# Performance work log

Hardware: AMD Instinct MI355X
Metric: run time of the kernel (lower is better)

## Reference

```python
import jax, jax.numpy as jnp
import numpy as np

HEADS = 4
DIM_HEAD = 32
GROUPS = 32  # min(256//4, 32)
EPS = 1e-5


def setup_inputs() -> dict:
    key = jax.random.key(0)
    ks = jax.random.split(key, 6)
    B, C, H, W = 16, 256, 64, 64
    hidden = HEADS * DIM_HEAD  # 128
    return {
        "x": jax.random.normal(ks[0], (B, C, H, W), dtype=jnp.float32),
        "gn_w": jax.random.uniform(ks[1], (C,), dtype=jnp.float32),
        "gn_b": jax.random.normal(ks[2], (C,), dtype=jnp.float32) * 0.05,
        "qkv_w": jax.random.normal(ks[3], (3 * hidden, C), dtype=jnp.float32) * 0.05,
        "qkv_b": jax.random.normal(ks[4], (3 * hidden,), dtype=jnp.float32) * 0.05,
        "out_w": jax.random.normal(ks[5], (C, hidden), dtype=jnp.float32) * 0.05,
        "out_b": jnp.zeros((C,), dtype=jnp.float32),
    }


def _forward_single(x, gn_w, gn_b, qkv_w, qkv_b, out_w, out_b):
    # x: (c, h, w)
    c, h, w = x.shape
    # GroupNorm over (channels-in-group, h, w)
    xg = x.reshape(GROUPS, c // GROUPS, h, w)
    mean = xg.mean(axis=(1, 2, 3), keepdims=True)
    var = xg.var(axis=(1, 2, 3), keepdims=True)
    xn = ((xg - mean) * jax.lax.rsqrt(var + EPS)).reshape(c, h, w)
    xn = xn * gn_w[:, None, None] + gn_b[:, None, None]
    # 1x1 conv QKV projection
    qkv = jnp.einsum('oc,chw->ohw', qkv_w, xn) + qkv_b[:, None, None]
    qkv = qkv.reshape(3, HEADS, DIM_HEAD, h * w)
    q, k, v = qkv[0], qkv[1], qkv[2]
    k = jax.nn.softmax(k, axis=-1)  # softmax over spatial
    context = jnp.einsum('hdn,hen->hde', k, v)   # (heads, d, d)
    out = jnp.einsum('hde,hdn->hen', context, q)  # (heads, d, n)
    out = out.reshape(HEADS * DIM_HEAD, h, w)
    # 1x1 conv output projection
    return jnp.einsum('oc,chw->ohw', out_w, out) + out_b[:, None, None]


def reference(x, gn_w, gn_b, qkv_w, qkv_b, out_w, out_b):
    f = lambda xi: _forward_single(xi, gn_w, gn_b, qkv_w, qkv_b, out_w, out_b)
    return jax.vmap(f)(x)
```

## Files before the change

kernel.cpp:

```cpp
#include <hip/hip_runtime.h>
#include <stdint.h>

typedef unsigned short u16;
typedef __attribute__((ext_vector_type(8))) short bf16x8;
typedef __attribute__((ext_vector_type(4))) float f32x4;

#define B_   16
#define C_   256
#define HW_  4096
#define QR_  384
#define HID_ 128

__device__ __forceinline__ float b2f(u16 u) {
  union { uint32_t i; float f; } v; v.i = ((uint32_t)u) << 16; return v.f;
}
__device__ __forceinline__ u16 f2b(float f) {
  union { float f; uint32_t i; } v; v.f = f;
  uint32_t r = (v.i + 0x7FFFu + ((v.i >> 16) & 1u)) >> 16;
  return (u16)r;
}

__global__ __launch_bounds__(256) void gn_stats_conv_kernel(
    const float* __restrict__ x, const float* __restrict__ gnw,
    const float* __restrict__ gnb, float* __restrict__ scale,
    float* __restrict__ shiftv,
    const float* __restrict__ qkvw, u16* __restrict__ cqkvw,
    u16* __restrict__ wqT)
{
  if (blockIdx.x >= 512) {
    int bi = blockIdx.x - 512;
    int t = threadIdx.x;
    if (bi < 96) {
      int i = bi * 256 + t;
      float4 f = ((const float4*)qkvw)[i];
      ushort4 o;
      o.x = f2b(f.x); o.y = f2b(f.y); o.z = f2b(f.z); o.w = f2b(f.w);
      ((ushort4*)cqkvw)[i] = o;
      return;
    }
    __shared__ u16 tl[16][272];
    for (int j = 0; j < 8; ++j) {
      int d = j * 16 + (t >> 4);
      int cb = (t & 15) * 16;
#pragma unroll
      for (int ii = 0; ii < 16; ++ii)
        tl[t >> 4][cb + ii] = f2b(qkvw[(size_t)d * 256 + cb + ii]);
      __syncthreads();
      union { u16 v[16]; uint4 q[2]; } pk;
#pragma unroll
      for (int dd = 0; dd < 16; ++dd) pk.v[dd] = tl[dd][t];
      *(uint4*)(wqT + (size_t)t * 128 + j * 16)     = pk.q[0];
      *(uint4*)(wqT + (size_t)t * 128 + j * 16 + 8) = pk.q[1];
      __syncthreads();
    }
    return;
  }
  int b = blockIdx.x >> 5, g = blockIdx.x & 31;
  const float* p = x + ((size_t)b * C_ + g * 8) * HW_;
  int t = threadIdx.x;
  float s = 0.f, sq = 0.f;
#pragma unroll
  for (int i = 0; i < 16; ++i) {
    float4 u0 = *(const float4*)(p + t * 8 + i * 2048);
    float4 u1 = *(const float4*)(p + t * 8 + i * 2048 + 4);
    s  += u0.x + u0.y + u0.z + u0.w + u1.x + u1.y + u1.z + u1.w;
    sq += u0.x*u0.x + u0.y*u0.y + u0.z*u0.z + u0.w*u0.w
        + u1.x*u1.x + u1.y*u1.y + u1.z*u1.z + u1.w*u1.w;
  }
#pragma unroll
  for (int off = 32; off > 0; off >>= 1) {
    s  += __shfl_down(s, off);
    sq += __shfl_down(sq, off);
  }
  __shared__ float ps[4], pq[4], mr[2];
  int lane = t & 63, w = t >> 6;
  if (lane == 0) { ps[w] = s; pq[w] = sq; }
  __syncthreads();
  if (t == 0) {
    float S = ps[0] + ps[1] + ps[2] + ps[3];
    float Q = pq[0] + pq[1] + pq[2] + pq[3];
    float mean = S * (1.f / 32768.f);
    float var  = Q * (1.f / 32768.f) - mean * mean;
    mr[0] = mean; mr[1] = rsqrtf(var + 1e-5f);
  }
  __syncthreads();
  if (t < 8) {
    int c = g * 8 + t;
    float sc = gnw[c] * mr[1];
    scale[b * C_ + c]  = sc;
    shiftv[b * C_ + c] = gnb[c] - mr[0] * sc;
  }
}

__global__ __launch_bounds__(256) void gn_transpose_kernel(
    const float* __restrict__ x, u16* __restrict__ dst,
    const float* __restrict__ scale, const float* __restrict__ shiftv)
{
  int nt = blockIdx.x, ct = blockIdx.y, b = blockIdx.z;
  const float* S = x + (size_t)b * C_ * HW_;
  u16* D = dst + (size_t)b * HW_ * C_;
  __shared__ __align__(16) u16 tile[64][136];
  int t = threadIdx.x;
  int n0 = nt * 128, c0 = ct * 64;
  int r = t >> 2, seg = (t & 3) * 32;
  float sc = scale[(size_t)b * C_ + c0 + r];
  float sh = shiftv[(size_t)b * C_ + c0 + r];
#pragma unroll
  for (int i = 0; i < 4; ++i) {
    const float* rp = S + (size_t)(c0 + r) * HW_ + n0 + seg + i * 8;
    float4 u0 = *(const float4*)(rp);
    float4 u1 = *(const float4*)(rp + 4);
    float f[8] = {u0.x, u0.y, u0.z, u0.w, u1.x, u1.y, u1.z, u1.w};
    uint4 o;
    uint32_t* op = (uint32_t*)&o;
#pragma unroll
    for (int j = 0; j < 4; ++j) {
      op[j] = (uint32_t)f2b(f[2 * j] * sc + sh)
            | ((uint32_t)f2b(f[2 * j + 1] * sc + sh) << 16);
    }
    *(uint4*)&tile[r][seg + i * 8] = o;
  }
  __syncthreads();
#pragma unroll
  for (int i = 0; i < 4; ++i) {
    int m = t * 4 + i;
    int n_l = m >> 3, cg = (m & 7) * 8;
    union { u16 v[8]; uint4 q; } pk;
#pragma unroll
    for (int e = 0; e < 8; ++e) pk.v[e] = tile[cg + e][n_l];
    *(uint4*)(D + (size_t)(n0 + n_l) * C_ + c0 + cg) = pk.q;
  }
}

__global__ __launch_bounds__(512) void kv_ctx_kernel(
    const u16* __restrict__ A,
    const u16* __restrict__ Bt,
    float* __restrict__ ctx_part,
    float* __restrict__ s_part)
{
  const int K = C_;
  int nt = blockIdx.x, b = blockIdx.y;
  const u16* Ab = A;
  const u16* Bb = Bt + (size_t)b * HW_ * C_ + (size_t)nt * 128 * K;
  __shared__ __align__(16) union {
    struct { u16 lA[256 * 64]; u16 lB[128 * 64]; } st;
    struct { u16 ek[128][136]; u16 vv[128][136]; float sred[2][128]; } ep;
    float cred[4096];
  } sm;
  int t = threadIdx.x;
  int lane = t & 63, w = t >> 6;
  int quad = lane >> 4, l16 = lane & 15;
  int wm = (w >> 1) * 64, wn = (w & 1) * 64;
  f32x4 acc[4][4];
#pragma unroll
  for (int i = 0; i < 4; ++i)
#pragma unroll
    for (int j = 0; j < 4; ++j)
#pragma unroll
      for (int r = 0; r < 4; ++r) acc[i][j][r] = 0.f;

  for (int k0 = 0; k0 < K; k0 += 64) {
    __syncthreads();
#pragma unroll
    for (int q = 0; q < 4; ++q) {
      int ch = q * 512 + t;
      int row = ch >> 3, off = (ch & 7) * 8;
      __builtin_amdgcn_global_load_lds(
          (const __attribute__((address_space(1))) void*)(Ab + (size_t)row * K + k0 + off),
          (__attribute__((address_space(3))) void*)(sm.st.lA + ch * 8), 16, 0, 0);
    }
#pragma unroll
    for (int q = 0; q < 2; ++q) {
      int ch = q * 512 + t;
      int row = ch >> 3, off = (ch & 7) * 8;
      __builtin_amdgcn_global_load_lds(
          (const __attribute__((address_space(1))) void*)(Bb + (size_t)row * K + k0 + off),
          (__attribute__((address_space(3))) void*)(sm.st.lB + ch * 8), 16, 0, 0);
    }
    __syncthreads();
    const bf16x8* A8 = (const bf16x8*)sm.st.lA;
    const bf16x8* B8 = (const bf16x8*)sm.st.lB;
#pragma unroll
    for (int kk = 0; kk < 2; ++kk) {
      bf16x8 af[4], bfr[4];
#pragma unroll
      for (int i = 0; i < 4; ++i) af[i]  = A8[(wm + i * 16 + l16) * 8 + kk * 4 + quad];
#pragma unroll
      for (int j = 0; j < 4; ++j) bfr[j] = B8[(wn + j * 16 + l16) * 8 + kk * 4 + quad];
#pragma unroll
      for (int i = 0; i < 4; ++i)
#pragma unroll
        for (int j = 0; j < 4; ++j)
          acc[i][j] = __builtin_amdgcn_mfma_f32_16x16x32_bf16(af[i], bfr[j],
                                                              acc[i][j], 0, 0, 0);
    }
  }

  __syncthreads();
  int h = w >> 1, nh = w & 1;
  if (w < 4) {
    float sl[4][4];
#pragma unroll
    for (int i = 0; i < 4; ++i)
#pragma unroll
      for (int r = 0; r < 4; ++r) sl[i][r] = 0.f;
#pragma unroll
    for (int i = 0; i < 4; ++i)
#pragma unroll
      for (int j = 0; j < 4; ++j)
#pragma unroll
        for (int r = 0; r < 4; ++r) {
          float e = __expf(acc[i][j][r]);
          sl[i][r] += e;
          sm.ep.ek[wm + i * 16 + quad * 4 + r][wn + j * 16 + l16] = f2b(e);
        }
#pragma unroll
    for (int i = 0; i < 4; ++i)
#pragma unroll
      for (int r = 0; r < 4; ++r) {
        float v = sl[i][r];
        v += __shfl_xor(v, 1);
        v += __shfl_xor(v, 2);
        v += __shfl_xor(v, 4);
        v += __shfl_xor(v, 8);
        if (l16 == 0) sm.ep.sred[nh][wm + i * 16 + quad * 4 + r] = v;
      }
  } else {
#pragma unroll
    for (int i = 0; i < 4; ++i)
#pragma unroll
      for (int j = 0; j < 4; ++j)
#pragma unroll
        for (int r = 0; r < 4; ++r)
          sm.ep.vv[wm - 128 + i * 16 + quad * 4 + r][wn + j * 16 + l16] =
              f2b(acc[i][j][r]);
  }
  __syncthreads();
  if (t < 128)
    s_part[((size_t)b * 32 + nt) * 128 + t] = sm.ep.sred[0][t] + sm.ep.sred[1][t];

  f32x4 c2[2][2];
#pragma unroll
  for (int i = 0; i < 2; ++i)
#pragma unroll
    for (int j = 0; j < 2; ++j)
#pragma unroll
      for (int r = 0; r < 4; ++r) c2[i][j][r] = 0.f;
#pragma unroll
  for (int kk = 0; kk < 2; ++kk) {
    bf16x8 ae[2], be[2];
#pragma unroll
    for (int i = 0; i < 2; ++i)
      ae[i] = *(const bf16x8*)&sm.ep.ek[h * 32 + i * 16 + l16][nh * 64 + kk * 32 + quad * 8];
#pragma unroll
    for (int j = 0; j < 2; ++j)
      be[j] = *(const bf16x8*)&sm.ep.vv[h * 32 + j * 16 + l16][nh * 64 + kk * 32 + quad * 8];
#pragma unroll
    for (int i = 0; i < 2; ++i)
#pragma unroll
      for (int j = 0; j < 2; ++j)
        c2[i][j] = __builtin_amdgcn_mfma_f32_16x16x32_bf16(ae[i], be[j], c2[i][j], 0, 0, 0);
  }
  __syncthreads();
  if (nh == 0) {
#pragma unroll
    for (int i = 0; i < 2; ++i)
#pragma unroll
      for (int j = 0; j < 2; ++j)
#pragma unroll
        for (int r = 0; r < 4; ++r)
          sm.cred[h * 1024 + (i * 16 + quad * 4 + r) * 32 + j * 16 + l16] = c2[i][j][r];
  }
  __syncthreads();
  if (nh == 1) {
#pragma unroll
    for (int i = 0; i < 2; ++i)
#pragma unroll
      for (int j = 0; j < 2; ++j)
#pragma unroll
        for (int r = 0; r < 4; ++r)
          sm.cred[h * 1024 + (i * 16 + quad * 4 + r) * 32 + j * 16 + l16] += c2[i][j][r];
  }
  __syncthreads();
  float4* dst = (float4*)(ctx_part + ((size_t)b * 32 + nt) * 4096);
  const float4* src4 = (const float4*)sm.cred;
  dst[t] = src4[t];
  dst[t + 512] = src4[t + 512];
}

__global__ __launch_bounds__(256) void fold_kernel(
    const float* __restrict__ ctx_part, const float* __restrict__ s_part,
    const float* __restrict__ outw, const float* __restrict__ qkvb,
    u16* __restrict__ wf, float* __restrict__ btp)
{
  int b = blockIdx.x >> 2, h = blockIdx.x & 3;
  int t = threadIdx.x;
  __shared__ float cs[1024];
  __shared__ float sinv[32];
  const float* cp = ctx_part + ((size_t)b * 32) * 4096 + h * 1024;
  float4 aa = make_float4(0.f, 0.f, 0.f, 0.f);
  for (int ntb = 0; ntb < 32; ++ntb) {
    float4 v = *(const float4*)(cp + (size_t)ntb * 4096 + t * 4);
    aa.x += v.x; aa.y += v.y; aa.z += v.z; aa.w += v.w;
  }
  *(float4*)&cs[t * 4] = aa;
  if (t < 32) {
    float ssum = 0.f;
    for (int ntb = 0; ntb < 32; ++ntb)
      ssum += s_part[((size_t)b * 32 + ntb) * 128 + h * 32 + t];
    sinv[t] = 1.f / ssum;
  }
  __syncthreads();
  int o = t;
  const float* wr = outw + (size_t)o * HID_ + h * 32;
  float wv[32];
  float cb = 0.f;
#pragma unroll
  for (int e = 0; e < 32; ++e) {
    wv[e] = wr[e];
    cb += wv[e] * qkvb[256 + h * 32 + e];
  }
  union { u16 v[32]; uint4 q[4]; } pk;
  float bacc = 0.f;
#pragma unroll
  for (int d = 0; d < 32; ++d) {
    float a = 0.f;
#pragma unroll
    for (int e = 0; e < 32; ++e) a += wv[e] * cs[d * 32 + e];
    float val = a * sinv[d] + cb;
    pk.v[d] = f2b(val);
    bacc += val * qkvb[h * 32 + d];
  }
  uint4* dp = (uint4*)(wf + ((size_t)b * C_ + o) * HID_ + h * 32);
#pragma unroll
  for (int i = 0; i < 4; ++i) dp[i] = pk.q[i];
  btp[((size_t)b * 4 + h) * 256 + o] = bacc;
}

__global__ __launch_bounds__(256) void out_gemm_kernel(
    const u16* __restrict__ wfp, const u16* __restrict__ wqT,
    const u16* __restrict__ Bt, const float* __restrict__ outb,
    const float* __restrict__ btp, float* __restrict__ Cout)
{
  int nt = blockIdx.x, mt = blockIdx.y, b = blockIdx.z;
  const u16* wfB = wfp + (size_t)b * C_ * HID_ + (size_t)mt * 128 * HID_;
  const u16* Bb  = Bt + (size_t)b * HW_ * C_ + (size_t)nt * 128 * C_;
  __shared__ __align__(16) u16 lWF[128 * 128];
  __shared__ __align__(16) u16 lWQ[64 * 128];
  __shared__ __align__(16) u16 lA[128 * 64];
  __shared__ __align__(16) u16 lB[128 * 64];
  int t = threadIdx.x;
  int lane = t & 63, w = t >> 6;
  int quad = lane >> 4, l16 = lane & 15;
  int wm = (w >> 1) * 64, wn = (w & 1) * 64;

#pragma unroll
  for (int q = 0; q < 8; ++q) {
    int ch = q * 256 + t;
    int row = ch >> 4, off = (ch & 15) * 8;
    __builtin_amdgcn_global_load_lds(
        (const __attribute__((address_space(1))) void*)(wfB + (size_t)row * HID_ + off),
        (__attribute__((address_space(3))) void*)(lWF + ch * 8), 16, 0, 0);
  }
  f32x4 acc[4][4];
#pragma unroll
  for (int i = 0; i < 4; ++i)
#pragma unroll
    for (int j = 0; j < 4; ++j)
#pragma unroll
      for (int r = 0; r < 4; ++r) acc[i][j][r] = 0.f;

  for (int k0 = 0; k0 < C_; k0 += 64) {
    __syncthreads();
#pragma unroll
    for (int q = 0; q < 4; ++q) {
      int ch = q * 256 + t;
      int row = ch >> 4, off = (ch & 15) * 8;
      __builtin_amdgcn_global_load_lds(
          (const __attribute__((address_space(1))) void*)(wqT + (size_t)(k0 + row) * HID_ + off),
          (__attribute__((address_space(3))) void*)(lWQ + ch * 8), 16, 0, 0);
    }
#pragma unroll
    for (int q = 0; q < 4; ++q) {
      int ch = q * 256 + t;
      int row = ch >> 3, off = (ch & 7) * 8;
      __builtin_amdgcn_global_load_lds(
          (const __attribute__((address_space(1))) void*)(Bb + (size_t)row * C_ + k0 + off),
          (__attribute__((address_space(3))) void*)(lB + ch * 8), 16, 0, 0);
    }
    __syncthreads();
    {
      f32x4 facc[2][4];
#pragma unroll
      for (int i2 = 0; i2 < 2; ++i2)
#pragma unroll
        for (int j2 = 0; j2 < 4; ++j2)
#pragma unroll
          for (int r = 0; r < 4; ++r) facc[i2][j2][r] = 0.f;
      const bf16x8* WF8 = (const bf16x8*)lWF;
      const bf16x8* WQ8 = (const bf16x8*)lWQ;
#pragma unroll
      for (int kk = 0; kk < 4; ++kk) {
        bf16x8 afv[2], bfv[4];
#pragma unroll
        for (int i2 = 0; i2 < 2; ++i2)
          afv[i2] = WF8[(w * 32 + i2 * 16 + l16) * 16 + kk * 4 + quad];
#pragma unroll
        for (int j2 = 0; j2 < 4; ++j2)
          bfv[j2] = WQ8[(j2 * 16 + l16) * 16 + kk * 4 + quad];
#pragma unroll
        for (int i2 = 0; i2 < 2; ++i2)
#pragma unroll
          for (int j2 = 0; j2 < 4; ++j2)
            facc[i2][j2] = __builtin_amdgcn_mfma_f32_16x16x32_bf16(
                afv[i2], bfv[j2], facc[i2][j2], 0, 0, 0);
      }
#pragma unroll
      for (int i2 = 0; i2 < 2; ++i2)
#pragma unroll
        for (int j2 = 0; j2 < 4; ++j2)
#pragma unroll
          for (int r = 0; r < 4; ++r)
            lA[(w * 32 + i2 * 16 + quad * 4 + r) * 64 + j2 * 16 + l16] =
                f2b(facc[i2][j2][r]);
    }
    __syncthreads();
    const bf16x8* A8 = (const bf16x8*)lA;
    const bf16x8* B8 = (const bf16x8*)lB;
#pragma unroll
    for (int kk = 0; kk < 2; ++kk) {
      bf16x8 af[4], bfr[4];
#pragma unroll
      for (int i = 0; i < 4; ++i) af[i]  = A8[(wm + i * 16 + l16) * 8 + kk * 4 + quad];
#pragma unroll
      for (int j = 0; j < 4; ++j) bfr[j] = B8[(wn + j * 16 + l16) * 8 + kk * 4 + quad];
#pragma unroll
      for (int i = 0; i < 4; ++i)
#pragma unroll
        for (int j = 0; j < 4; ++j)
          acc[i][j] = __builtin_amdgcn_mfma_f32_16x16x32_bf16(af[i], bfr[j],
                                                              acc[i][j], 0, 0, 0);
    }
  }
#pragma unroll
  for (int i = 0; i < 4; ++i) {
#pragma unroll
    for (int rg = 0; rg < 4; ++rg) {
      int o = mt * 128 + wm + i * 16 + quad * 4 + rg;
      float bsv = outb[o]
                + btp[((size_t)b * 4 + 0) * 256 + o]
                + btp[((size_t)b * 4 + 1) * 256 + o]
                + btp[((size_t)b * 4 + 2) * 256 + o]
                + btp[((size_t)b * 4 + 3) * 256 + o];
      size_t rowbase = (size_t)b * C_ * HW_ + (size_t)o * HW_;
#pragma unroll
      for (int j = 0; j < 4; ++j) {
        int n = nt * 128 + wn + j * 16 + l16;
        Cout[rowbase + n] = acc[i][j][rg] + bsv;
      }
    }
  }
}

extern "C" void kernel_launch(void* const* d_in, const int* in_sizes, int n_in,
                              void* d_out, int out_size, void* d_ws, size_t ws_size,
                              hipStream_t stream)
{
  const float* x    = (const float*)d_in[0];
  const float* gnw  = (const float*)d_in[1];
  const float* gnb  = (const float*)d_in[2];
  const float* qkvw = (const float*)d_in[3];
  const float* qkvb = (const float*)d_in[4];
  const float* outw = (const float*)d_in[5];
  const float* outb = (const float*)d_in[6];

  char* p = (char*)d_ws;
  float* scale  = (float*)p;            p += (size_t)B_ * C_ * 4;
  float* shiftv = (float*)p;            p += (size_t)B_ * C_ * 4;
  u16* cqkvw = (u16*)p;                 p += (size_t)QR_ * C_ * 2;
  u16* wqT   = (u16*)p;                 p += (size_t)C_ * HID_ * 2;
  u16* xn_t  = (u16*)p;                 p += (size_t)B_ * HW_ * C_ * 2;
  u16* wf    = (u16*)p;                 p += (size_t)B_ * C_ * HID_ * 2;
  float* ctxp = (float*)p;              p += (size_t)B_ * 32 * 4 * 1024 * 4;
  float* sp   = (float*)p;              p += (size_t)B_ * 32 * 128 * 4;
  float* btp  = (float*)p;

  gn_stats_conv_kernel<<<609, 256, 0, stream>>>(x, gnw, gnb, scale, shiftv,
                                                qkvw, cqkvw, wqT);
  gn_transpose_kernel<<<dim3(32, 4, 16), 256, 0, stream>>>(x, xn_t, scale, shiftv);
  kv_ctx_kernel<<<dim3(32, 16), 512, 0, stream>>>(cqkvw + 128 * C_, xn_t, ctxp, sp);
  fold_kernel<<<64, 256, 0, stream>>>(ctxp, sp, outw, qkvb, wf, btp);
  out_gemm_kernel<<<dim3(32, 2, 16), 256, 0, stream>>>(wf, wqT, xn_t, outb, btp,
                                                       (float*)d_out);
}
```

Before: 214.9 us.

## Precompute per-batch combined weight in separate GEMM instead of recomputing per tile

After: 195.1 us. -9.2%, faster.

```diff
diff --git a/kernel.cpp b/kernel.cpp
--- a/kernel.cpp
+++ b/kernel.cpp
@@ -337,31 +337,20 @@
   btp[((size_t)b * 4 + h) * 256 + o] = bacc;
 }
 
-__global__ __launch_bounds__(256) void out_gemm_kernel(
+__global__ __launch_bounds__(256) void wtot_gemm_kernel(
     const u16* __restrict__ wfp, const u16* __restrict__ wqT,
-    const u16* __restrict__ Bt, const float* __restrict__ outb,
-    const float* __restrict__ btp, float* __restrict__ Cout)
-{
+    u16* __restrict__ wtot)
+{
+  const int K = HID_;
   int nt = blockIdx.x, mt = blockIdx.y, b = blockIdx.z;
-  const u16* wfB = wfp + (size_t)b * C_ * HID_ + (size_t)mt * 128 * HID_;
-  const u16* Bb  = Bt + (size_t)b * HW_ * C_ + (size_t)nt * 128 * C_;
-  __shared__ __align__(16) u16 lWF[128 * 128];
-  __shared__ __align__(16) u16 lWQ[64 * 128];
+  const u16* Ab = wfp + (size_t)b * C_ * HID_ + (size_t)mt * 128 * K;
+  const u16* Bb = wqT + (size_t)nt * 128 * K;
   __shared__ __align__(16) u16 lA[128 * 64];
   __shared__ __align__(16) u16 lB[128 * 64];
   int t = threadIdx.x;
   int lane = t & 63, w = t >> 6;
   int quad = lane >> 4, l16 = lane & 15;
   int wm = (w >> 1) * 64, wn = (w & 1) * 64;
-
-#pragma unroll
-  for (int q = 0; q < 8; ++q) {
-    int ch = q * 256 + t;
-    int row = ch >> 4, off = (ch & 15) * 8;
-    __builtin_amdgcn_global_load_lds(
-        (const __attribute__((address_space(1))) void*)(wfB + (size_t)row * HID_ + off),
-        (__attribute__((address_space(3))) void*)(lWF + ch * 8), 16, 0, 0);
-  }
   f32x4 acc[4][4];
 #pragma unroll
   for (int i = 0; i < 4; ++i)
@@ -370,59 +359,87 @@
 #pragma unroll
       for (int r = 0; r < 4; ++r) acc[i][j][r] = 0.f;
 
-  for (int k0 = 0; k0 < C_; k0 += 64) {
+  for (int k0 = 0; k0 < K; k0 += 64) {
     __syncthreads();
-#pragma unroll
-    for (int q = 0; q < 4; ++q) {
-      int ch = q * 256 + t;
-      int row = ch >> 4, off = (ch & 15) * 8;
-      __builtin_amdgcn_global_load_lds(
-          (const __attribute__((address_space(1))) void*)(wqT + (size_t)(k0 + row) * HID_ + off),
-          (__attribute__((address_space(3))) void*)(lWQ + ch * 8), 16, 0, 0);
-    }
 #pragma unroll
     for (int q = 0; q < 4; ++q) {
       int ch = q * 256 + t;
       int row = ch >> 3, off = (ch & 7) * 8;
       __builtin_amdgcn_global_load_lds(
-          (const __attribute__((address_space(1))) void*)(Bb + (size_t)row * C_ + k0 + off),
+          (const __attribute__((address_space(1))) void*)(Ab + (size_t)row * K + k0 + off),
+          (__attribute__((address_space(3))) void*)(lA + ch * 8), 16, 0, 0);
+      __builtin_amdgcn_global_load_lds(
+          (const __attribute__((address_space(1))) void*)(Bb + (size_t)row * K + k0 + off),
           (__attribute__((address_space(3))) void*)(lB + ch * 8), 16, 0, 0);
     }
     __syncthreads();
-    {
-      f32x4 facc[2][4];
-#pragma unroll
-      for (int i2 = 0; i2 < 2; ++i2)
-#pragma unroll
-        for (int j2 = 0; j2 < 4; ++j2)
-#pragma unroll
-          for (int r = 0; r < 4; ++r) facc[i2][j2][r] = 0.f;
-      const bf16x8* WF8 = (const bf16x8*)lWF;
-      const bf16x8* WQ8 = (const bf16x8*)lWQ;
-#pragma unroll
-      for (int kk = 0; kk < 4; ++kk) {
-        bf16x8 afv[2], bfv[4];
-#pragma unroll
-        for (int i2 = 0; i2 < 2; ++i2)
-          afv[i2] = WF8[(w * 32 + i2 * 16 + l16) * 16 + kk * 4 + quad];
-#pragma unroll
-        for (int j2 = 0; j2 < 4; ++j2)
-          bfv[j2] = WQ8[(j2 * 16 + l16) * 16 + kk * 4 + quad];
-#pragma unroll
-        for (int i2 = 0; i2 < 2; ++i2)
-#pragma unroll
-          for (int j2 = 0; j2 < 4; ++j2)
-            facc[i2][j2] = __builtin_amdgcn_mfma_f32_16x16x32_bf16(
-                afv[i2], bfv[j2], facc[i2][j2], 0, 0, 0);
+    const bf16x8* A8 = (const bf16x8*)lA;
+    const bf16x8* B8 = (const bf16x8*)lB;
+#pragma unroll
+    for (int kk = 0; kk < 2; ++kk) {
+      bf16x8 af[4], bfr[4];
+#pragma unroll
+      for (int i = 0; i < 4; ++i) af[i]  = A8[(wm + i * 16 + l16) * 8 + kk * 4 + quad];
+#pragma unroll
+      for (int j = 0; j < 4; ++j) bfr[j] = B8[(wn + j * 16 + l16) * 8 + kk * 4 + quad];
+#pragma unroll
+      for (int i = 0; i < 4; ++i)
+#pragma unroll
+        for (int j = 0; j < 4; ++j)
+          acc[i][j] = __builtin_amdgcn_mfma_f32_16x16x32_bf16(af[i], bfr[j],
+                                                              acc[i][j], 0, 0, 0);
+    }
+  }
+  u16* Wb = wtot + (size_t)b * C_ * C_;
+#pragma unroll
+  for (int i = 0; i < 4; ++i) {
+#pragma unroll
+    for (int rg = 0; rg < 4; ++rg) {
+      int o = mt * 128 + wm + i * 16 + quad * 4 + rg;
+#pragma unroll
+      for (int j = 0; j < 4; ++j) {
+        int c = nt * 128 + wn + j * 16 + l16;
+        Wb[(size_t)o * C_ + c] = f2b(acc[i][j][rg]);
       }
-#pragma unroll
-      for (int i2 = 0; i2 < 2; ++i2)
-#pragma unroll
-        for (int j2 = 0; j2 < 4; ++j2)
-#pragma unroll
-          for (int r = 0; r < 4; ++r)
-            lA[(w * 32 + i2 * 16 + quad * 4 + r) * 64 + j2 * 16 + l16] =
-                f2b(facc[i2][j2][r]);
+    }
+  }
+}
+
+__global__ __launch_bounds__(256) void out_gemm_kernel(
+    const u16* __restrict__ wtot, const u16* __restrict__ Bt,
+    const float* __restrict__ outb, const float* __restrict__ btp,
+    float* __restrict__ Cout)
+{
+  const int K = C_;
+  int nt = blockIdx.x, mt = blockIdx.y, b = blockIdx.z;
+  const u16* Ab = wtot + (size_t)b * C_ * C_ + (size_t)mt * 128 * K;
+  const u16* Bb = Bt + (size_t)b * HW_ * C_ + (size_t)nt * 128 * K;
+  __shared__ __align__(16) u16 lA[128 * 64];
+  __shared__ __align__(16) u16 lB[128 * 64];
+  int t = threadIdx.x;
+  int lane = t & 63, w = t >> 6;
+  int quad = lane >> 4, l16 = lane & 15;
+  int wm = (w >> 1) * 64, wn = (w & 1) * 64;
+  f32x4 acc[4][4];
+#pragma unroll
+  for (int i = 0; i < 4; ++i)
+#pragma unroll
+    for (int j = 0; j < 4; ++j)
+#pragma unroll
+      for (int r = 0; r < 4; ++r) acc[i][j][r] = 0.f;
+
+  for (int k0 = 0; k0 < K; k0 += 64) {
+    __syncthreads();
+#pragma unroll
+    for (int q = 0; q < 4; ++q) {
+      int ch = q * 256 + t;
+      int row = ch >> 3, off = (ch & 7) * 8;
+      __builtin_amdgcn_global_load_lds(
+          (const __attribute__((address_space(1))) void*)(Ab + (size_t)row * K + k0 + off),
+          (__attribute__((address_space(3))) void*)(lA + ch * 8), 16, 0, 0);
+      __builtin_amdgcn_global_load_lds(
+          (const __attribute__((address_space(1))) void*)(Bb + (size_t)row * K + k0 + off),
+          (__attribute__((address_space(3))) void*)(lB + ch * 8), 16, 0, 0);
     }
     __syncthreads();
     const bf16x8* A8 = (const bf16x8*)lA;
@@ -481,6 +498,7 @@
   u16* wqT   = (u16*)p;                 p += (size_t)C_ * HID_ * 2;
   u16* xn_t  = (u16*)p;                 p += (size_t)B_ * HW_ * C_ * 2;
   u16* wf    = (u16*)p;                 p += (size_t)B_ * C_ * HID_ * 2;
+  u16* wtot  = (u16*)p;                 p += (size_t)B_ * C_ * C_ * 2;
   float* ctxp = (float*)p;              p += (size_t)B_ * 32 * 4 * 1024 * 4;
   float* sp   = (float*)p;              p += (size_t)B_ * 32 * 128 * 4;
   float* btp  = (float*)p;
@@ -490,6 +508,7 @@
   gn_transpose_kernel<<<dim3(32, 4, 16), 256, 0, stream>>>(x, xn_t, scale, shiftv);
   kv_ctx_kernel<<<dim3(32, 16), 512, 0, stream>>>(cqkvw + 128 * C_, xn_t, ctxp, sp);
   fold_kernel<<<64, 256, 0, stream>>>(ctxp, sp, outw, qkvb, wf, btp);
-  out_gemm_kernel<<<dim3(32, 2, 16), 256, 0, stream>>>(wf, wqT, xn_t, outb, btp,
+  wtot_gemm_kernel<<<dim3(2, 2, 16), 256, 0, stream>>>(wf, wqT, wtot);
+  out_gemm_kernel<<<dim3(32, 2, 16), 256, 0, stream>>>(wtot, xn_t, outb, btp,
                                                        (float*)d_out);
 }
```
